# Kernel optimization log

Hardware: AMD Instinct MI355X
Metric: run time of the kernel (lower is better)

The kernel has to match this reference:

```python
import jax, jax.numpy as jnp
import numpy as np

NBOXES = 4096
MAX_BS = 128
NDIM = 3
NPAIRS = 8192
INV4PI = 0.07957747154594767  # 1/(4*pi), 3D Laplace kernel constant


def setup_inputs() -> dict:
    key = jax.random.key(0)
    k1, k2, k3, k4 = jax.random.split(key, 4)
    q_vec = jax.random.normal(k1, (NBOXES, MAX_BS), dtype=jnp.float32)
    XX_list = jax.random.uniform(k2, (NBOXES, MAX_BS, NDIM), dtype=jnp.float32)
    bs_list = jax.random.randint(k3, (NBOXES,), 0, MAX_BS, dtype=jnp.int32)
    uq_boxes = jax.random.randint(k4, (NPAIRS, 2), 0, NBOXES, dtype=jnp.int32)
    return {"q_vec": q_vec, "XX_list": XX_list, "bs_list": bs_list, "uq_boxes": uq_boxes}


def reference(q_vec, XX_list, bs_list, uq_boxes):
    # Batched gather-kernel-matvec-scatter translation (addto_translation with
    # self_bool=False, kappa=0 => 3D Laplace kernel 1/(4*pi*r)).
    nboxes, max_bs = q_vec.shape
    u_boxes = uq_boxes[:, 0]
    q_boxes = uq_boxes[:, 1]

    Xu = XX_list[u_boxes]  # [P, B, 3] gather target points
    Xq = XX_list[q_boxes]  # [P, B, 3] gather source points

    # pairwise squared distances without materializing [P,B,B,3] diffs
    nu = jnp.sum(Xu * Xu, axis=-1)  # [P, B]
    nq = jnp.sum(Xq * Xq, axis=-1)  # [P, B]
    r2 = nu[:, :, None] + nq[:, None, :] - 2.0 * jnp.einsum('pid,pjd->pij', Xu, Xq)
    r2 = jnp.maximum(r2, 0.0)
    nz = r2 > 0.0
    K = jnp.where(nz, INV4PI / jnp.sqrt(jnp.where(nz, r2, 1.0)), 0.0)  # [P, B, B]

    cols = jnp.arange(max_bs, dtype=jnp.int32)
    col_mask = (cols[None, :] < bs_list[q_boxes][:, None]).astype(q_vec.dtype)  # valid src pts
    row_mask = (cols[None, :] < bs_list[u_boxes][:, None]).astype(q_vec.dtype)  # valid trg pts

    qv = q_vec[q_boxes] * col_mask                         # gather + zero_col_bnd
    out = jnp.einsum('pij,pj->pi', K, qv) * row_mask       # batched kernel matvec

    u_vec = jnp.zeros_like(q_vec).at[u_boxes].add(out)     # index_add_ scatter
    return u_vec
```

## Files before the change

kernel.cpp:

```cpp
#include <hip/hip_runtime.h>

#define NBOXES 4096
#define MAX_BS 128
#define INV4PI 0.07957747154594767f

__global__ __launch_bounds__(128) void fmm_pair_kernel(
    const float* __restrict__ q_vec,
    const float* __restrict__ XX,
    const int*   __restrict__ bs_list,
    const int2*  __restrict__ uq_boxes,
    float*       __restrict__ out)
{
    const int p = blockIdx.x;
    const int t = threadIdx.x;

    const int2 uq = uq_boxes[p];
    const int u = uq.x;
    const int q = uq.y;
    const int bs_u = bs_list[u];
    const int bs_q = bs_list[q];

    __shared__ float4 sq[MAX_BS];

    {
        const float* Xq = XX + (size_t)q * (MAX_BS * 3);
        float x = Xq[3 * t + 0];
        float y = Xq[3 * t + 1];
        float z = Xq[3 * t + 2];
        float w = (t < bs_q) ? q_vec[(size_t)q * MAX_BS + t] * INV4PI : 0.0f;
        sq[t] = make_float4(x, y, z, w);
    }

    const float* Xu = XX + (size_t)u * (MAX_BS * 3);
    const float xu = Xu[3 * t + 0];
    const float yu = Xu[3 * t + 1];
    const float zu = Xu[3 * t + 2];

    __syncthreads();

    if (t >= bs_u) return;

    float acc = 0.0f;
    const int n = bs_q;
#pragma unroll 4
    for (int j = 0; j < n; ++j) {
        const float4 s = sq[j];
        const float dx = xu - s.x;
        const float dy = yu - s.y;
        const float dz = zu - s.z;
        const float r2 = dx * dx + dy * dy + dz * dz;
        float rinv = __builtin_amdgcn_rsqf(r2);
        rinv = (r2 > 0.0f) ? rinv : 0.0f;
        acc = fmaf(s.w, rinv, acc);
    }

    atomicAdd(out + (size_t)u * MAX_BS + t, acc);
}

extern "C" void kernel_launch(void* const* d_in, const int* in_sizes, int n_in,
                              void* d_out, int out_size, void* d_ws, size_t ws_size,
                              hipStream_t stream) {
    const float* q_vec    = (const float*)d_in[0];
    const float* XX_list  = (const float*)d_in[1];
    const int*   bs_list  = (const int*)d_in[2];
    const int2*  uq_boxes = (const int2*)d_in[3];
    float* out = (float*)d_out;

    const int npairs = in_sizes[3] / 2;

    hipMemsetAsync(d_out, 0, (size_t)out_size * sizeof(float), stream);

    fmm_pair_kernel<<<npairs, 128, 0, stream>>>(q_vec, XX_list, bs_list,
                                                uq_boxes, out);
}
```

Baseline: 89.15 us.

## Replace LDS staging with wave-uniform scalar loads of source points

Box indices are made wave-uniform with readfirstlane, so source coordinates and charges can be read straight from global memory through the scalar load path. This removes the shared-memory staging and the block barrier, and adds an early exit for inactive threads and empty source boxes. When u != q it drops the r2>0 guard, which assumes no coincident points across different boxes. The 1/(4π) scale moves to a single multiply before the atomic. The risk is scalar-load latency in the inner loop, which the 8-way unroll is meant to hide.

```diff
diff --git a/kernel.cpp b/kernel.cpp
--- a/kernel.cpp
+++ b/kernel.cpp
@@ -1,10 +1,9 @@
 #include <hip/hip_runtime.h>
 
-#define NBOXES 4096
 #define MAX_BS 128
 #define INV4PI 0.07957747154594767f
 
-__global__ __launch_bounds__(128) void fmm_pair_kernel(
+__global__ __launch_bounds__(128) void fmm_scalar_kernel(
     const float* __restrict__ q_vec,
     const float* __restrict__ XX,
     const int*   __restrict__ bs_list,
@@ -15,46 +14,53 @@
     const int t = threadIdx.x;
 
     const int2 uq = uq_boxes[p];
-    const int u = uq.x;
-    const int q = uq.y;
+    const int u = __builtin_amdgcn_readfirstlane(uq.x);
+    const int q = __builtin_amdgcn_readfirstlane(uq.y);
     const int bs_u = bs_list[u];
     const int bs_q = bs_list[q];
 
-    __shared__ float4 sq[MAX_BS];
+    if (t >= bs_u || bs_q == 0) return;
 
-    {
-        const float* Xq = XX + (size_t)q * (MAX_BS * 3);
-        float x = Xq[3 * t + 0];
-        float y = Xq[3 * t + 1];
-        float z = Xq[3 * t + 2];
-        float w = (t < bs_q) ? q_vec[(size_t)q * MAX_BS + t] * INV4PI : 0.0f;
-        sq[t] = make_float4(x, y, z, w);
-    }
-
-    const float* Xu = XX + (size_t)u * (MAX_BS * 3);
+    const float* __restrict__ Xu = XX + (size_t)u * (MAX_BS * 3);
     const float xu = Xu[3 * t + 0];
     const float yu = Xu[3 * t + 1];
     const float zu = Xu[3 * t + 2];
 
-    __syncthreads();
-
-    if (t >= bs_u) return;
+    const float* __restrict__ Xq = XX + (size_t)q * (MAX_BS * 3);
+    const float* __restrict__ qv = q_vec + (size_t)q * MAX_BS;
 
     float acc = 0.0f;
-    const int n = bs_q;
+    if (u != q) {
+#pragma unroll 8
+        for (int j = 0; j < bs_q; ++j) {
+            const float sx = Xq[3 * j + 0];
+            const float sy = Xq[3 * j + 1];
+            const float sz = Xq[3 * j + 2];
+            const float w  = qv[j];
+            const float dx = xu - sx;
+            const float dy = yu - sy;
+            const float dz = zu - sz;
+            const float r2 = dx * dx + dy * dy + dz * dz;
+            acc = fmaf(w, __builtin_amdgcn_rsqf(r2), acc);
+        }
+    } else {
 #pragma unroll 4
-    for (int j = 0; j < n; ++j) {
-        const float4 s = sq[j];
-        const float dx = xu - s.x;
-        const float dy = yu - s.y;
-        const float dz = zu - s.z;
-        const float r2 = dx * dx + dy * dy + dz * dz;
-        float rinv = __builtin_amdgcn_rsqf(r2);
-        rinv = (r2 > 0.0f) ? rinv : 0.0f;
-        acc = fmaf(s.w, rinv, acc);
+        for (int j = 0; j < bs_q; ++j) {
+            const float sx = Xq[3 * j + 0];
+            const float sy = Xq[3 * j + 1];
+            const float sz = Xq[3 * j + 2];
+            const float w  = qv[j];
+            const float dx = xu - sx;
+            const float dy = yu - sy;
+            const float dz = zu - sz;
+            const float r2 = dx * dx + dy * dy + dz * dz;
+            float rinv = __builtin_amdgcn_rsqf(r2);
+            rinv = (r2 > 0.0f) ? rinv : 0.0f;
+            acc = fmaf(w, rinv, acc);
+        }
     }
 
-    atomicAdd(out + (size_t)u * MAX_BS + t, acc);
+    atomicAdd(out + (size_t)u * MAX_BS + t, acc * INV4PI);
 }
 
 extern "C" void kernel_launch(void* const* d_in, const int* in_sizes, int n_in,
@@ -70,6 +76,6 @@
 
     hipMemsetAsync(d_out, 0, (size_t)out_size * sizeof(float), stream);
 
-    fmm_pair_kernel<<<npairs, 128, 0, stream>>>(q_vec, XX_list, bs_list,
-                                                uq_boxes, out);
+    fmm_scalar_kernel<<<npairs, 128, 0, stream>>>(
+        q_vec, XX_list, bs_list, uq_boxes, out);
 }
```

Measured after the change: 85.97 us. 3.6% less time.

## Prepack source points into paired SoA layout and use packed-FMA inner loop

Applied to the files above, without the earlier changes.

Adds a prep kernel that repacks every box's source coordinates and pre-scaled masked charges into pairs of points stored as {x0,x1,y0,y1,z0,z1,w0,w1} in workspace. The pair kernel drops shared memory and the barrier, reads the packed data straight from global/L2 as uniform loads, and processes two sources per iteration with 2-wide vector FMAs, which can map to packed math. The r2>0 check is kept only on the u==q path, on the assumption that distinct boxes never have coincident points. This adds an extra launch and workspace traffic, and makes every thread issue its own loads instead of reading from LDS.

```diff
diff --git a/kernel.cpp b/kernel.cpp
--- a/kernel.cpp
+++ b/kernel.cpp
@@ -2,56 +2,86 @@
 
 #define NBOXES 4096
 #define MAX_BS 128
+#define NPTS (NBOXES * MAX_BS)
 #define INV4PI 0.07957747154594767f
 
-__global__ __launch_bounds__(128) void fmm_pair_kernel(
-    const float* __restrict__ q_vec,
+typedef float v2f __attribute__((ext_vector_type(2)));
+
+__global__ __launch_bounds__(256) void prep_kernel(
+    const float* __restrict__ XX, const float* __restrict__ q_vec,
+    const int* __restrict__ bs_list, float4* __restrict__ pk)
+{
+    const int g = blockIdx.x * 256 + threadIdx.x;
+    const int b = g >> 6;
+    const int j = (g & 63) * 2;
+    const float* X = XX + (size_t)b * (MAX_BS * 3) + 3 * j;
+    const float x0 = X[0], y0 = X[1], z0 = X[2];
+    const float x1 = X[3], y1 = X[4], z1 = X[5];
+    const int bs = bs_list[b];
+    const float* qv = q_vec + (size_t)b * MAX_BS + j;
+    const float w0 = (j     < bs) ? qv[0] * INV4PI : 0.0f;
+    const float w1 = (j + 1 < bs) ? qv[1] * INV4PI : 0.0f;
+    pk[2 * g + 0] = make_float4(x0, x1, y0, y1);
+    pk[2 * g + 1] = make_float4(z0, z1, w0, w1);
+}
+
+__global__ __launch_bounds__(128) void fmm_packed_kernel(
     const float* __restrict__ XX,
     const int*   __restrict__ bs_list,
     const int2*  __restrict__ uq_boxes,
+    const v2f*   __restrict__ pk,
     float*       __restrict__ out)
 {
     const int p = blockIdx.x;
     const int t = threadIdx.x;
 
     const int2 uq = uq_boxes[p];
-    const int u = uq.x;
-    const int q = uq.y;
+    const int u = __builtin_amdgcn_readfirstlane(uq.x);
+    const int q = __builtin_amdgcn_readfirstlane(uq.y);
     const int bs_u = bs_list[u];
+    if (t >= bs_u) return;
     const int bs_q = bs_list[q];
+    const int ng = (bs_q + 1) >> 1;
 
-    __shared__ float4 sq[MAX_BS];
+    const float* __restrict__ Xu = XX + (size_t)u * (MAX_BS * 3) + 3 * t;
+    const float xu = Xu[0], yu = Xu[1], zu = Xu[2];
 
-    {
-        const float* Xq = XX + (size_t)q * (MAX_BS * 3);
-        float x = Xq[3 * t + 0];
-        float y = Xq[3 * t + 1];
-        float z = Xq[3 * t + 2];
-        float w = (t < bs_q) ? q_vec[(size_t)q * MAX_BS + t] * INV4PI : 0.0f;
-        sq[t] = make_float4(x, y, z, w);
-    }
-
-    const float* Xu = XX + (size_t)u * (MAX_BS * 3);
-    const float xu = Xu[3 * t + 0];
-    const float yu = Xu[3 * t + 1];
-    const float zu = Xu[3 * t + 2];
-
-    __syncthreads();
-
-    if (t >= bs_u) return;
+    const v2f* __restrict__ pq = pk + (size_t)q * (MAX_BS * 2);
 
     float acc = 0.0f;
-    const int n = bs_q;
+    if (u != q) {
+        const v2f xup = {xu, xu}, yup = {yu, yu}, zup = {zu, zu};
+        v2f accp = {0.0f, 0.0f};
 #pragma unroll 4
-    for (int j = 0; j < n; ++j) {
-        const float4 s = sq[j];
-        const float dx = xu - s.x;
-        const float dy = yu - s.y;
-        const float dz = zu - s.z;
-        const float r2 = dx * dx + dy * dy + dz * dz;
-        float rinv = __builtin_amdgcn_rsqf(r2);
-        rinv = (r2 > 0.0f) ? rinv : 0.0f;
-        acc = fmaf(s.w, rinv, acc);
+        for (int k = 0; k < ng; ++k) {
+            const v2f sx = pq[4 * k + 0];
+            const v2f sy = pq[4 * k + 1];
+            const v2f sz = pq[4 * k + 2];
+            const v2f sw = pq[4 * k + 3];
+            const v2f dx = xup - sx;
+            const v2f dy = yup - sy;
+            const v2f dz = zup - sz;
+            v2f r2 = dx * dx;
+            r2 = __builtin_elementwise_fma(dy, dy, r2);
+            r2 = __builtin_elementwise_fma(dz, dz, r2);
+            v2f rv;
+            rv.x = __builtin_amdgcn_rsqf(r2.x);
+            rv.y = __builtin_amdgcn_rsqf(r2.y);
+            accp = __builtin_elementwise_fma(sw, rv, accp);
+        }
+        acc = accp.x + accp.y;
+    } else {
+        for (int j = 0; j < bs_q; ++j) {
+            const float* g = (const float*)(pq + 4 * (j >> 1));
+            const int o = j & 1;
+            const float sx = g[0 + o], sy = g[2 + o];
+            const float sz = g[4 + o], sw = g[6 + o];
+            const float dx = xu - sx, dy = yu - sy, dz = zu - sz;
+            const float r2 = fmaf(dx, dx, fmaf(dy, dy, dz * dz));
+            float rv = __builtin_amdgcn_rsqf(r2);
+            rv = (r2 > 0.0f) ? rv : 0.0f;
+            acc = fmaf(sw, rv, acc);
+        }
     }
 
     atomicAdd(out + (size_t)u * MAX_BS + t, acc);
@@ -68,8 +98,13 @@
 
     const int npairs = in_sizes[3] / 2;
 
+    float4* pk = (float4*)d_ws;
+
     hipMemsetAsync(d_out, 0, (size_t)out_size * sizeof(float), stream);
 
-    fmm_pair_kernel<<<npairs, 128, 0, stream>>>(q_vec, XX_list, bs_list,
-                                                uq_boxes, out);
+    prep_kernel<<<(NPTS / 2) / 256, 256, 0, stream>>>(
+        XX_list, q_vec, bs_list, pk);
+
+    fmm_packed_kernel<<<npairs, 128, 0, stream>>>(
+        XX_list, bs_list, uq_boxes, (const v2f*)pk, out);
 }
```

After: 86.93 us. -2.5%, faster.
